# Performance work log

Hardware: AMD Instinct MI355X
Metric: run time of the kernel (lower is better)

## Reference

```python
import jax, jax.numpy as jnp
import numpy as np

B = 65536
IN_DIM = 1280
E = 8          # num_experts
H1 = 256       # hidden_dim
H2 = 128       # hidden_dim // 2


def setup_inputs() -> dict:
    key = jax.random.key(0)
    ks = jax.random.split(key, 9)
    s1 = 1.0 / np.sqrt(IN_DIM)
    s2 = 1.0 / np.sqrt(H1)
    s3 = 1.0 / np.sqrt(H2)
    return {
        "x":  jax.random.normal(ks[0], (B, IN_DIM), dtype=jnp.float32),
        # stacked expert params: layer1 [E,in,H1], layer2 [E,H1,H2], layer3 [E,H2]
        "W1": jax.random.uniform(ks[1], (E, IN_DIM, H1), jnp.float32, -s1, s1),
        "b1": jax.random.uniform(ks[2], (E, H1), jnp.float32, -s1, s1),
        "W2": jax.random.uniform(ks[3], (E, H1, H2), jnp.float32, -s2, s2),
        "b2": jax.random.uniform(ks[4], (E, H2), jnp.float32, -s2, s2),
        "W3": jax.random.uniform(ks[5], (E, H2), jnp.float32, -s3, s3),
        "b3": jax.random.uniform(ks[6], (E,), jnp.float32, -s3, s3),
        # gate params [in,E]
        "Wg": jax.random.uniform(ks[7], (IN_DIM, E), jnp.float32, -s1, s1),
        "bg": jax.random.uniform(ks[8], (E,), jnp.float32, -s1, s1),
    }


def reference(x, W1, b1, W2, b2, W3, b3, Wg, bg):
    # All E experts run densely on every token (dropout = eval/identity).
    h1 = jax.nn.relu(jnp.einsum("bi,eih->beh", x, W1) + b1)          # [B,E,H1]
    h2 = jax.nn.relu(jnp.einsum("beh,ehk->bek", h1, W2) + b2)        # [B,E,H2]
    expert_out = jnp.einsum("bek,ek->be", h2, W3) + b3               # [B,E]
    gate = jax.nn.softmax(x @ Wg + bg, axis=-1)                      # [B,E]
    predictions = jnp.sum(expert_out * gate, axis=1)                 # [B]
    return predictions, gate
```

## Files before the change

### kernel.cpp

```cpp
#include <hip/hip_runtime.h>
#include <stdint.h>

#define NTOK 65536
#define KDIM 1280

typedef __attribute__((ext_vector_type(8))) short short8;
typedef __attribute__((ext_vector_type(4))) float floatx4;

__device__ __forceinline__ unsigned short f2bf(float f) {
  union { float f; unsigned int u; } v; v.f = f;
  unsigned int r = v.u + 0x7FFFu + ((v.u >> 16) & 1u);
  return (unsigned short)(r >> 16);
}

#define GLDS16(gp, lp) \
  __builtin_amdgcn_global_load_lds((const __attribute__((address_space(1))) void*)(gp), \
                                   (__attribute__((address_space(3))) void*)(lp), 16, 0, 0)


__global__ __launch_bounds__(256) void cast_x_kernel(const float4* __restrict__ x,
                                                     uint2* __restrict__ xb) {
  size_t i = (size_t)blockIdx.x * 256 + threadIdx.x;
  float4 v = x[i];
  uint2 o;
  o.x = (unsigned)f2bf(v.x) | ((unsigned)f2bf(v.y) << 16);
  o.y = (unsigned)f2bf(v.z) | ((unsigned)f2bf(v.w) << 16);
  xb[i] = o;
}

__global__ __launch_bounds__(256) void pack_w1_kernel(const float* __restrict__ W1,
                                                      unsigned short* __restrict__ W1t) {
  int t = blockIdx.x * 256 + threadIdx.x;
  if (t >= 2048 * 160) return;
  int n = t / 160, kg = t - n * 160;
  int e = n >> 8, h = n & 255;
  int k = kg * 8;
  const float* src = W1 + ((size_t)e * 1280 + k) * 256 + h;
  uint4 o;
  o.x = (unsigned)f2bf(src[0])       | ((unsigned)f2bf(src[256])     << 16);
  o.y = (unsigned)f2bf(src[2 * 256]) | ((unsigned)f2bf(src[3 * 256]) << 16);
  o.z = (unsigned)f2bf(src[4 * 256]) | ((unsigned)f2bf(src[5 * 256]) << 16);
  o.w = (unsigned)f2bf(src[6 * 256]) | ((unsigned)f2bf(src[7 * 256]) << 16);
  *(uint4*)(W1t + (size_t)n * 1280 + k) = o;
}

__global__ __launch_bounds__(256) void pack_w2_kernel(const float* __restrict__ W2,
                                                      unsigned short* __restrict__ W2t) {
  int t = blockIdx.x * 256 + threadIdx.x;
  if (t >= 1024 * 32) return;
  int ng = t >> 5, kg = t & 31;
  int e = ng >> 7, n = ng & 127;
  int k = kg * 8;
  const float* src = W2 + (size_t)e * 32768 + (size_t)k * 128 + n;
  uint4 o;
  o.x = (unsigned)f2bf(src[0])       | ((unsigned)f2bf(src[128])     << 16);
  o.y = (unsigned)f2bf(src[2 * 128]) | ((unsigned)f2bf(src[3 * 128]) << 16);
  o.z = (unsigned)f2bf(src[4 * 128]) | ((unsigned)f2bf(src[5 * 128]) << 16);
  o.w = (unsigned)f2bf(src[6 * 128]) | ((unsigned)f2bf(src[7 * 128]) << 16);
  *(uint4*)(W2t + (size_t)ng * 256 + k) = o;
}

__global__ __launch_bounds__(256) void pack_wg_kernel(const float* __restrict__ Wg,
                                                      unsigned short* __restrict__ WgTb) {
  int t = blockIdx.x * 256 + threadIdx.x;
  if (t >= 16 * 1280) return;
  int e = t / 1280, k = t - e * 1280;
  WgTb[t] = (e < 8) ? f2bf(Wg[(size_t)k * 8 + e]) : (unsigned short)0;
}


__global__ __launch_bounds__(256, 3)
void expert_fused_kernel(const unsigned short* __restrict__ xb,
                         const unsigned short* __restrict__ W1t,
                         const float* __restrict__ b1,
                         const unsigned short* __restrict__ W2t,
                         const float* __restrict__ b2,
                         const float* __restrict__ W3,
                         const float* __restrict__ b3,
                         const unsigned short* __restrict__ WgTb,
                         const float* __restrict__ bg,
                         float* __restrict__ outG,
                         float* __restrict__ eo) {
  __shared__ __align__(16) unsigned short smem[24576];
  unsigned short* WsA = smem;
  unsigned short* WsB = smem + 8192;
  unsigned short* XsA = smem + 16384;
  unsigned short* XsB = smem + 18432;
  unsigned short* h1L = smem;
  unsigned short* W2A = smem + 16384;
  unsigned short* W2B = smem + 20480;
  unsigned short* WgA = smem + 20480;
  unsigned short* WgB = smem + 21504;

  const int tid = threadIdx.x;
  const int wv = tid >> 6;
  const int lane = tid & 63;
  const int e = blockIdx.x;
  const int m0 = blockIdx.y << 6;
  const bool gate_blk = (e == 0);

  const unsigned short* W1te = W1t + (size_t)e * 256 * 1280;
  const unsigned short* W2te = W2t + (size_t)e * 128 * 256;

  const int lr = lane >> 2;
  const int ksw = ((lane & 3) ^ ((lane >> 3) & 3)) * 8;
  const int fr = lane & 15;
  const int fkS = (((lane >> 4) ^ ((lane >> 1) & 3)) & 3) * 8;
  const int fkL = (lane >> 4) * 8;
  const int rq = (lane >> 4) * 4;

  const unsigned short* gx = xb + (size_t)(m0 + wv * 16 + lr) * 1280 + ksw;
  const unsigned short* gw = W1te + (size_t)(wv * 64 + lr) * 1280 + ksw;
  const unsigned short* gwg = WgTb + (size_t)lr * 1280 + ksw;
  unsigned short* lxA = &XsA[(wv * 16) * 32];
  unsigned short* lxB = &XsB[(wv * 16) * 32];
  unsigned short* lwA = &WsA[(wv * 64) * 32];
  unsigned short* lwB = &WsB[(wv * 64) * 32];
  const bool gate_stager = gate_blk && (wv == 0);

  floatx4 acc1[4][4] = {};
  floatx4 accg = {0.f, 0.f, 0.f, 0.f};
  for (int k0 = 0; k0 < 1280; k0 += 64) {
    GLDS16(gx + k0, lxA);
    GLDS16(gx + k0 + 32, lxB);
#pragma unroll
    for (int r = 0; r < 4; r++) {
      GLDS16(gw + (size_t)(16 * r) * 1280 + k0, lwA + r * 16 * 32);
      GLDS16(gw + (size_t)(16 * r) * 1280 + k0 + 32, lwB + r * 16 * 32);
    }
    if (gate_stager) { GLDS16(gwg + k0, WgA); GLDS16(gwg + k0 + 32, WgB); }
    __syncthreads();
    {
      short8 bfv[4];
#pragma unroll
      for (int j = 0; j < 4; j++)
        bfv[j] = *(const short8*)&XsA[(j * 16 + fr) * 32 + fkS];
#pragma unroll
      for (int i = 0; i < 4; i++) {
        short8 af = *(const short8*)&WsA[(wv * 64 + i * 16 + fr) * 32 + fkS];
#pragma unroll
        for (int j = 0; j < 4; j++)
          acc1[i][j] = __builtin_amdgcn_mfma_f32_16x16x32_bf16(af, bfv[j], acc1[i][j], 0, 0, 0);
      }
      if (gate_blk) {
        short8 ag = *(const short8*)&WgA[fr * 32 + fkS];
        short8 bgf = *(const short8*)&XsA[(wv * 16 + fr) * 32 + fkS];
        accg = __builtin_amdgcn_mfma_f32_16x16x32_bf16(ag, bgf, accg, 0, 0, 0);
      }
    }
    {
      short8 bfv[4];
#pragma unroll
      for (int j = 0; j < 4; j++)
        bfv[j] = *(const short8*)&XsB[(j * 16 + fr) * 32 + fkS];
#pragma unroll
      for (int i = 0; i < 4; i++) {
        short8 af = *(const short8*)&WsB[(wv * 64 + i * 16 + fr) * 32 + fkS];
#pragma unroll
        for (int j = 0; j < 4; j++)
          acc1[i][j] = __builtin_amdgcn_mfma_f32_16x16x32_bf16(af, bfv[j], acc1[i][j], 0, 0, 0);
      }
      if (gate_blk) {
        short8 ag = *(const short8*)&WgB[fr * 32 + fkS];
        short8 bgf = *(const short8*)&XsB[(wv * 16 + fr) * 32 + fkS];
        accg = __builtin_amdgcn_mfma_f32_16x16x32_bf16(ag, bgf, accg, 0, 0, 0);
      }
    }
    __syncthreads();
  }

  if (gate_blk) {
    const int g = lane >> 4;
    float bg0 = 0.f, bg1 = 0.f, bg2 = 0.f, bg3 = 0.f;
    if (g < 2) {
      float4 t = *(const float4*)(bg + g * 4);
      bg0 = t.x; bg1 = t.y; bg2 = t.z; bg3 = t.w;
    }
    float v0 = accg[0] + bg0, v1 = accg[1] + bg1, v2 = accg[2] + bg2, v3 = accg[3] + bg3;
    float mx = fmaxf(fmaxf(v0, v1), fmaxf(v2, v3));
    mx = fmaxf(mx, __shfl_xor(mx, 16));
    float e0 = __expf(v0 - mx), e1 = __expf(v1 - mx), e2 = __expf(v2 - mx), e3 = __expf(v3 - mx);
    float s = e0 + e1 + e2 + e3;
    s += __shfl_xor(s, 16);
    float inv = 1.f / s;
    if (g < 2) {
      float4 o; o.x = e0 * inv; o.y = e1 * inv; o.z = e2 * inv; o.w = e3 * inv;
      *(float4*)&outG[(size_t)(m0 + wv * 16 + fr) * 8 + g * 4] = o;
    }
  }

#pragma unroll
  for (int i = 0; i < 4; i++) {
    const int rowb = wv * 64 + i * 16 + rq;
    const float4 bb = *(const float4*)(b1 + e * 256 + rowb);
#pragma unroll
    for (int j = 0; j < 4; j++) {
      float v0 = acc1[i][j][0] + bb.x; v0 = v0 > 0.f ? v0 : 0.f;
      float v1 = acc1[i][j][1] + bb.y; v1 = v1 > 0.f ? v1 : 0.f;
      float v2 = acc1[i][j][2] + bb.z; v2 = v2 > 0.f ? v2 : 0.f;
      float v3 = acc1[i][j][3] + bb.w; v3 = v3 > 0.f ? v3 : 0.f;
      uint2 pk;
      pk.x = (unsigned)f2bf(v0) | ((unsigned)f2bf(v1) << 16);
      pk.y = (unsigned)f2bf(v2) | ((unsigned)f2bf(v3) << 16);
      const int row = j * 16 + fr;
      *(uint2*)((char*)h1L + ((row * 512 + rowb * 2) ^ ((row & 7) << 4))) = pk;
    }
  }
  __syncthreads();

  floatx4 acc2[2][4] = {};
  const unsigned short* gw2 = W2te + (size_t)(wv * 32 + lr) * 256 + ksw;
  unsigned short* lw2A = &W2A[(wv * 32) * 32];
  unsigned short* lw2B = &W2B[(wv * 32) * 32];
  for (int k0 = 0; k0 < 256; k0 += 64) {
    GLDS16(gw2 + k0, lw2A);
    GLDS16(gw2 + 16 * 256 + k0, lw2A + 16 * 32);
    GLDS16(gw2 + k0 + 32, lw2B);
    GLDS16(gw2 + 16 * 256 + k0 + 32, lw2B + 16 * 32);
    __syncthreads();
#pragma unroll
    for (int h = 0; h < 2; h++) {
      const unsigned short* W2s = h ? W2B : W2A;
      const int kk = k0 + h * 32;
      short8 b2v[4];
#pragma unroll
      for (int j = 0; j < 4; j++) {
        const int row = j * 16 + fr;
        b2v[j] = *(const short8*)((const char*)h1L +
                 ((row * 512 + (kk + fkL) * 2) ^ ((row & 7) << 4)));
      }
#pragma unroll
      for (int i = 0; i < 2; i++) {
        short8 a2 = *(const short8*)&W2s[(wv * 32 + i * 16 + fr) * 32 + fkS];
#pragma unroll
        for (int j = 0; j < 4; j++)
          acc2[i][j] = __builtin_amdgcn_mfma_f32_16x16x32_bf16(a2, b2v[j], acc2[i][j], 0, 0, 0);
      }
    }
    __syncthreads();
  }

  float psum[4] = {0.f, 0.f, 0.f, 0.f};
#pragma unroll
  for (int i = 0; i < 2; i++) {
    const int rowb = wv * 32 + i * 16 + rq;
    const float4 bb = *(const float4*)(b2 + e * 128 + rowb);
    const float4 ww = *(const float4*)(W3 + e * 128 + rowb);
    const float bba[4] = {bb.x, bb.y, bb.z, bb.w};
    const float wwa[4] = {ww.x, ww.y, ww.z, ww.w};
#pragma unroll
    for (int j = 0; j < 4; j++)
#pragma unroll
      for (int r = 0; r < 4; r++) {
        float v = acc2[i][j][r] + bba[r];
        v = v > 0.f ? v : 0.f;
        psum[j] += v * wwa[r];
      }
  }
#pragma unroll
  for (int j = 0; j < 4; j++) {
    float v = psum[j];
    v += __shfl_xor(v, 16);
    v += __shfl_xor(v, 32);
    psum[j] = v;
  }
  float* exS = (float*)XsA;
  if (lane < 16) {
#pragma unroll
    for (int j = 0; j < 4; j++) exS[wv * 64 + j * 16 + lane] = psum[j];
  }
  __syncthreads();
  if (tid < 64) {
    float tot = exS[tid] + exS[64 + tid] + exS[128 + tid] + exS[192 + tid];
    eo[(size_t)(m0 + tid) * 8 + e] = tot + b3[e];
  }
}


__global__ __launch_bounds__(256)
void combine_kernel(const float* __restrict__ outG, const float* __restrict__ eo,
                    float* __restrict__ outP) {
  int t = blockIdx.x * 256 + threadIdx.x;
  const float4* g4 = (const float4*)(outG + (size_t)t * 8);
  const float4* e4 = (const float4*)(eo + (size_t)t * 8);
  float4 ga = g4[0], gb = g4[1], ea = e4[0], eb = e4[1];
  outP[t] = ga.x * ea.x + ga.y * ea.y + ga.z * ea.z + ga.w * ea.w +
            gb.x * eb.x + gb.y * eb.y + gb.z * eb.z + gb.w * eb.w;
}


extern "C" void kernel_launch(void* const* d_in, const int* in_sizes, int n_in,
                              void* d_out, int out_size, void* d_ws, size_t ws_size,
                              hipStream_t stream) {
  const float* x  = (const float*)d_in[0];
  const float* W1 = (const float*)d_in[1];
  const float* b1 = (const float*)d_in[2];
  const float* W2 = (const float*)d_in[3];
  const float* b2 = (const float*)d_in[4];
  const float* W3 = (const float*)d_in[5];
  const float* b3 = (const float*)d_in[6];
  const float* Wg = (const float*)d_in[7];
  const float* bg = (const float*)d_in[8];
  float* outP = (float*)d_out;
  float* outG = outP + NTOK;

  char* ws = (char*)d_ws;
  unsigned short* xb   = (unsigned short*)ws;
  unsigned short* W1t  = (unsigned short*)(ws + 167772160ll);
  unsigned short* W2t  = (unsigned short*)(ws + 173015040ll);
  unsigned short* WgTb = (unsigned short*)(ws + 173539328ll);
  float*          eo   = (float*)(ws + 173580288ll);

  cast_x_kernel<<<NTOK * KDIM / 4 / 256, 256, 0, stream>>>((const float4*)x, (uint2*)xb);
  pack_w1_kernel<<<1280, 256, 0, stream>>>(W1, W1t);
  pack_w2_kernel<<<128, 256, 0, stream>>>(W2, W2t);
  pack_wg_kernel<<<80, 256, 0, stream>>>(Wg, WgTb);

  expert_fused_kernel<<<dim3(8, 1024), 256, 0, stream>>>(xb, W1t, b1, W2t, b2, W3, b3,
                                                         WgTb, bg, outG, eo);
  combine_kernel<<<256, 256, 0, stream>>>(outG, eo, outP);
}
```

Measured before the change: 902.0 us.

## Fuse x bf16 cast into expert GEMM loads, merge weight packing kernels, remap blocks

Drops the separate x-to-bf16 cast kernel, which wrote a 160MB bf16 copy that the GEMM then read back. The GEMM now loads fp32 x directly, converts it in registers with v_cvt_pk_bf16_f32 and writes it to LDS. The three weight-pack kernels are merged into one launch. Blocks are remapped so the 8 experts sharing a token tile are scheduled near each other, to improve L2 reuse of x. In exchange, x global traffic per block doubles (fp32), each block repeats the conversion, and synchronous register loads replace async LDS DMA for x.

```diff
diff --git a/kernel.cpp b/kernel.cpp
--- a/kernel.cpp
+++ b/kernel.cpp
@@ -13,64 +13,56 @@
   return (unsigned short)(r >> 16);
 }
 
+__device__ __forceinline__ unsigned cvtpk(float lo, float hi) {
+  unsigned r;
+  asm("v_cvt_pk_bf16_f32 %0, %1, %2" : "=v"(r) : "v"(lo), "v"(hi));
+  return r;
+}
+
 #define GLDS16(gp, lp) \
   __builtin_amdgcn_global_load_lds((const __attribute__((address_space(1))) void*)(gp), \
                                    (__attribute__((address_space(3))) void*)(lp), 16, 0, 0)
 
 
-__global__ __launch_bounds__(256) void cast_x_kernel(const float4* __restrict__ x,
-                                                     uint2* __restrict__ xb) {
-  size_t i = (size_t)blockIdx.x * 256 + threadIdx.x;
-  float4 v = x[i];
-  uint2 o;
-  o.x = (unsigned)f2bf(v.x) | ((unsigned)f2bf(v.y) << 16);
-  o.y = (unsigned)f2bf(v.z) | ((unsigned)f2bf(v.w) << 16);
-  xb[i] = o;
-}
-
-__global__ __launch_bounds__(256) void pack_w1_kernel(const float* __restrict__ W1,
-                                                      unsigned short* __restrict__ W1t) {
+__global__ __launch_bounds__(256)
+void pack_all_kernel(const float* __restrict__ W1, const float* __restrict__ W2,
+                     const float* __restrict__ Wg,
+                     unsigned short* __restrict__ W1t, unsigned short* __restrict__ W2t,
+                     unsigned short* __restrict__ WgTb) {
   int t = blockIdx.x * 256 + threadIdx.x;
-  if (t >= 2048 * 160) return;
-  int n = t / 160, kg = t - n * 160;
-  int e = n >> 8, h = n & 255;
-  int k = kg * 8;
-  const float* src = W1 + ((size_t)e * 1280 + k) * 256 + h;
-  uint4 o;
-  o.x = (unsigned)f2bf(src[0])       | ((unsigned)f2bf(src[256])     << 16);
-  o.y = (unsigned)f2bf(src[2 * 256]) | ((unsigned)f2bf(src[3 * 256]) << 16);
-  o.z = (unsigned)f2bf(src[4 * 256]) | ((unsigned)f2bf(src[5 * 256]) << 16);
-  o.w = (unsigned)f2bf(src[6 * 256]) | ((unsigned)f2bf(src[7 * 256]) << 16);
-  *(uint4*)(W1t + (size_t)n * 1280 + k) = o;
-}
-
-__global__ __launch_bounds__(256) void pack_w2_kernel(const float* __restrict__ W2,
-                                                      unsigned short* __restrict__ W2t) {
-  int t = blockIdx.x * 256 + threadIdx.x;
-  if (t >= 1024 * 32) return;
-  int ng = t >> 5, kg = t & 31;
-  int e = ng >> 7, n = ng & 127;
-  int k = kg * 8;
-  const float* src = W2 + (size_t)e * 32768 + (size_t)k * 128 + n;
-  uint4 o;
-  o.x = (unsigned)f2bf(src[0])       | ((unsigned)f2bf(src[128])     << 16);
-  o.y = (unsigned)f2bf(src[2 * 128]) | ((unsigned)f2bf(src[3 * 128]) << 16);
-  o.z = (unsigned)f2bf(src[4 * 128]) | ((unsigned)f2bf(src[5 * 128]) << 16);
-  o.w = (unsigned)f2bf(src[6 * 128]) | ((unsigned)f2bf(src[7 * 128]) << 16);
-  *(uint4*)(W2t + (size_t)ng * 256 + k) = o;
-}
-
-__global__ __launch_bounds__(256) void pack_wg_kernel(const float* __restrict__ Wg,
-                                                      unsigned short* __restrict__ WgTb) {
-  int t = blockIdx.x * 256 + threadIdx.x;
-  if (t >= 16 * 1280) return;
-  int e = t / 1280, k = t - e * 1280;
-  WgTb[t] = (e < 8) ? f2bf(Wg[(size_t)k * 8 + e]) : (unsigned short)0;
+  if (t < 327680) {
+    int n = t / 160, kg = t - n * 160;
+    int e = n >> 8, h = n & 255;
+    int k = kg * 8;
+    const float* src = W1 + ((size_t)e * 1280 + k) * 256 + h;
+    uint4 o;
+    o.x = (unsigned)f2bf(src[0])       | ((unsigned)f2bf(src[256])     << 16);
+    o.y = (unsigned)f2bf(src[2 * 256]) | ((unsigned)f2bf(src[3 * 256]) << 16);
+    o.z = (unsigned)f2bf(src[4 * 256]) | ((unsigned)f2bf(src[5 * 256]) << 16);
+    o.w = (unsigned)f2bf(src[6 * 256]) | ((unsigned)f2bf(src[7 * 256]) << 16);
+    *(uint4*)(W1t + (size_t)n * 1280 + k) = o;
+  } else if (t < 360448) {
+    int t2 = t - 327680;
+    int ng = t2 >> 5, kg = t2 & 31;
+    int e = ng >> 7, n = ng & 127;
+    int k = kg * 8;
+    const float* src = W2 + (size_t)e * 32768 + (size_t)k * 128 + n;
+    uint4 o;
+    o.x = (unsigned)f2bf(src[0])       | ((unsigned)f2bf(src[128])     << 16);
+    o.y = (unsigned)f2bf(src[2 * 128]) | ((unsigned)f2bf(src[3 * 128]) << 16);
+    o.z = (unsigned)f2bf(src[4 * 128]) | ((unsigned)f2bf(src[5 * 128]) << 16);
+    o.w = (unsigned)f2bf(src[6 * 128]) | ((unsigned)f2bf(src[7 * 128]) << 16);
+    *(uint4*)(W2t + (size_t)ng * 256 + k) = o;
+  } else {
+    int t3 = t - 360448;
+    int e = t3 / 1280, k = t3 - e * 1280;
+    WgTb[t3] = (e < 8) ? f2bf(Wg[(size_t)k * 8 + e]) : (unsigned short)0;
+  }
 }
 
 
 __global__ __launch_bounds__(256, 3)
-void expert_fused_kernel(const unsigned short* __restrict__ xb,
+void expert_fused_kernel(const float* __restrict__ xf,
                          const unsigned short* __restrict__ W1t,
                          const float* __restrict__ b1,
                          const unsigned short* __restrict__ W2t,
@@ -95,8 +87,12 @@
   const int tid = threadIdx.x;
   const int wv = tid >> 6;
   const int lane = tid & 63;
-  const int e = blockIdx.x;
-  const int m0 = blockIdx.y << 6;
+
+  const int wg = blockIdx.x + (blockIdx.y << 3);
+  const int c  = wg & 7;
+  const int w  = wg >> 3;
+  const int e  = w & 7;
+  const int m0 = ((c << 7) + (w >> 3)) << 6;
   const bool gate_blk = (e == 0);
 
   const unsigned short* W1te = W1t + (size_t)e * 256 * 1280;
@@ -109,11 +105,9 @@
   const int fkL = (lane >> 4) * 8;
   const int rq = (lane >> 4) * 4;
 
-  const unsigned short* gx = xb + (size_t)(m0 + wv * 16 + lr) * 1280 + ksw;
+  const float* gxf = xf + (size_t)(m0 + wv * 16 + lr) * 1280 + ksw;
   const unsigned short* gw = W1te + (size_t)(wv * 64 + lr) * 1280 + ksw;
   const unsigned short* gwg = WgTb + (size_t)lr * 1280 + ksw;
-  unsigned short* lxA = &XsA[(wv * 16) * 32];
-  unsigned short* lxB = &XsB[(wv * 16) * 32];
   unsigned short* lwA = &WsA[(wv * 64) * 32];
   unsigned short* lwB = &WsB[(wv * 64) * 32];
   const bool gate_stager = gate_blk && (wv == 0);
@@ -121,14 +115,23 @@
   floatx4 acc1[4][4] = {};
   floatx4 accg = {0.f, 0.f, 0.f, 0.f};
   for (int k0 = 0; k0 < 1280; k0 += 64) {
-    GLDS16(gx + k0, lxA);
-    GLDS16(gx + k0 + 32, lxB);
+    float4 xa0 = *(const float4*)(gxf + k0);
+    float4 xa1 = *(const float4*)(gxf + k0 + 4);
+    float4 xb0 = *(const float4*)(gxf + k0 + 32);
+    float4 xb1 = *(const float4*)(gxf + k0 + 36);
 #pragma unroll
     for (int r = 0; r < 4; r++) {
       GLDS16(gw + (size_t)(16 * r) * 1280 + k0, lwA + r * 16 * 32);
       GLDS16(gw + (size_t)(16 * r) * 1280 + k0 + 32, lwB + r * 16 * 32);
     }
     if (gate_stager) { GLDS16(gwg + k0, WgA); GLDS16(gwg + k0 + 32, WgB); }
+    uint4 pa, pb;
+    pa.x = cvtpk(xa0.x, xa0.y); pa.y = cvtpk(xa0.z, xa0.w);
+    pa.z = cvtpk(xa1.x, xa1.y); pa.w = cvtpk(xa1.z, xa1.w);
+    pb.x = cvtpk(xb0.x, xb0.y); pb.y = cvtpk(xb0.z, xb0.w);
+    pb.z = cvtpk(xb1.x, xb1.y); pb.w = cvtpk(xb1.z, xb1.w);
+    *(uint4*)&XsA[(wv * 16 + lr) * 32 + (lane & 3) * 8] = pa;
+    *(uint4*)&XsB[(wv * 16 + lr) * 32 + (lane & 3) * 8] = pb;
     __syncthreads();
     {
       short8 bfv[4];
@@ -305,18 +308,13 @@
   float* outG = outP + NTOK;
 
   char* ws = (char*)d_ws;
-  unsigned short* xb   = (unsigned short*)ws;
-  unsigned short* W1t  = (unsigned short*)(ws + 167772160ll);
-  unsigned short* W2t  = (unsigned short*)(ws + 173015040ll);
-  unsigned short* WgTb = (unsigned short*)(ws + 173539328ll);
-  float*          eo   = (float*)(ws + 173580288ll);
-
-  cast_x_kernel<<<NTOK * KDIM / 4 / 256, 256, 0, stream>>>((const float4*)x, (uint2*)xb);
-  pack_w1_kernel<<<1280, 256, 0, stream>>>(W1, W1t);
-  pack_w2_kernel<<<128, 256, 0, stream>>>(W2, W2t);
-  pack_wg_kernel<<<80, 256, 0, stream>>>(Wg, WgTb);
-
-  expert_fused_kernel<<<dim3(8, 1024), 256, 0, stream>>>(xb, W1t, b1, W2t, b2, W3, b3,
+  unsigned short* W1t  = (unsigned short*)ws;
+  unsigned short* W2t  = (unsigned short*)(ws + 5242880ll);
+  unsigned short* WgTb = (unsigned short*)(ws + 5767168ll);
+  float*          eo   = (float*)(ws + 5808128ll);
+
+  pack_all_kernel<<<1488, 256, 0, stream>>>(W1, W2, Wg, W1t, W2t, WgTb);
+  expert_fused_kernel<<<dim3(8, 1024), 256, 0, stream>>>(x, W1t, b1, W2t, b2, W3, b3,
                                                          WgTb, bg, outG, eo);
   combine_kernel<<<256, 256, 0, stream>>>(outG, eo, outP);
 }
```

New measurement: 890.4 us. No clear change (-1.3%).
